# Optimization experiments

Measured on AMD Instinct MI355X. Metric: run time of the kernel, lower is better.

## Reference

```python
import jax, jax.numpy as jnp
import numpy as np
import itertools

W_ASSIGN = 1.0   # options_file['assignments_loss_weight']
W_CAT = 0.5      # options_file['categorizer_loss_weight']


def _bce(p, y):
    # torch.nn.BCELoss semantics: log terms clamped at -100
    logp = jnp.clip(jnp.log(p), -100.0)
    log1mp = jnp.clip(jnp.log1p(-p), -100.0)
    return -(y * logp + (1.0 - y) * log1mp)


def setup_inputs() -> dict:
    key = jax.random.key(0)
    k0, k1, k2, k3 = jax.random.split(key, 4)
    B, P, M = 8192, 4, 12
    assignments = jax.random.uniform(k0, (B, P, M, M), dtype=jnp.float32)
    category = jax.random.uniform(k1, (B, P), dtype=jnp.float32)
    assignments_labels = jax.random.randint(k2, (B, P, M, M), 0, 2).astype(jnp.float32)
    category_labels = jax.random.randint(k3, (B, P), 0, 2).astype(jnp.float32)
    return {
        "assignments": assignments,
        "category": category,
        "assignments_labels": assignments_labels,
        "category_labels": category_labels,
    }


def reference(assignments, category, assignments_labels, category_labels):
    B, P = assignments.shape[0], assignments.shape[1]
    # All P! permutations, in itertools order (matches first-strict-min tie-break
    # of the original loop combined with argmin's first-occurrence rule).
    perms = jnp.asarray(np.array(list(itertools.permutations(range(P))), dtype=np.int32))  # [K, P]

    # [B, K, P, M, M]: assignments with slot dim permuted for every permutation
    permuted = assignments[:, perms]
    elem = _bce(permuted, assignments_labels[:, None])          # [B, K, P, M, M]
    per_perm_loss = elem.mean(axis=(2, 3, 4))                   # [B, K]

    min_loss = per_perm_loss.min(axis=1)                        # [B]
    best = jnp.argmin(per_perm_loss, axis=1)                    # [B]
    batch_perms = perms[best]                                   # [B, P]

    permuted_category = jnp.take_along_axis(category, batch_perms, axis=1)  # [B, P]

    assignments_loss = min_loss.mean()
    category_loss = _bce(permuted_category, category_labels).mean()
    return W_ASSIGN * assignments_loss + W_CAT * category_loss
```

## Files before the change

kernel.cpp:

```cpp
#include <hip/hip_runtime.h>
#include <math.h>


#define LOG2_CLIP (-144.26950408889634f)
#define LN2F      (0.6931471805599453f)

#define PK(a,b,c,d) ((unsigned)((4u*(a)) | ((16u+4u*(b))<<8) | \
                                ((32u+4u*(c))<<16) | ((48u+4u*(d))<<24)))
__device__ const unsigned PERM_PK[32] = {
    PK(0,1,2,3), PK(0,1,3,2), PK(0,2,1,3), PK(0,2,3,1), PK(0,3,1,2), PK(0,3,2,1),
    PK(1,0,2,3), PK(1,0,3,2), PK(1,2,0,3), PK(1,2,3,0), PK(1,3,0,2), PK(1,3,2,0),
    PK(2,0,1,3), PK(2,0,3,1), PK(2,1,0,3), PK(2,1,3,0), PK(2,3,0,1), PK(2,3,1,0),
    PK(3,0,1,2), PK(3,0,2,1), PK(3,1,0,2), PK(3,1,2,0), PK(3,2,0,1), PK(3,2,1,0),
    PK(0,1,2,3), PK(0,1,2,3), PK(0,1,2,3), PK(0,1,2,3),
    PK(0,1,2,3), PK(0,1,2,3), PK(0,1,2,3), PK(0,1,2,3)
};

__global__ __launch_bounds__(256) void hsl_per_batch(
    const float* __restrict__ assign,
    const float* __restrict__ cat,
    const float* __restrict__ alabels,
    const float* __restrict__ clabels,
    float* __restrict__ ws,
    int B)
{
    const int wave = (int)((blockIdx.x * blockDim.x + threadIdx.x) >> 6);
    const int lane = (int)(threadIdx.x & 63);
    if (wave >= B) return;
    const int b = wave;

    const float* __restrict__ A = assign  + (size_t)b * 576;
    const float* __restrict__ Y = alabels + (size_t)b * 576;

    float s[16], T[4];
#pragma unroll
    for (int i = 0; i < 16; ++i) s[i] = 0.0f;
#pragma unroll
    for (int i = 0; i < 4; ++i) T[i] = 0.0f;

#pragma unroll
    for (int it = 0; it < 3; ++it) {
        if (it < 2 || lane < 16) {
            const int e = lane + it * 64;
            float d[4], y[4];
#pragma unroll
            for (int q = 0; q < 4; ++q) {
                const float a  = A[q * 144 + e];
                const float la = fmaxf(__log2f(a),        LOG2_CLIP);
                const float lb = fmaxf(__log2f(1.0f - a), LOG2_CLIP);
                d[q] = la - lb;
                T[q] += lb;
            }
#pragma unroll
            for (int p = 0; p < 4; ++p) y[p] = Y[p * 144 + e];
#pragma unroll
            for (int p = 0; p < 4; ++p)
#pragma unroll
                for (int q = 0; q < 4; ++q)
                    s[p * 4 + q] = fmaf(y[p], d[q], s[p * 4 + q]);
        }
    }
#pragma unroll
    for (int i = 0; i < 16; ++i) s[i] += T[i & 3];

    const bool h32 = (lane & 32) != 0;
    const bool h16 = (lane & 16) != 0;
    const bool h8  = (lane & 8)  != 0;
    const bool h4  = (lane & 4)  != 0;

    float t[8];
#pragma unroll
    for (int i = 0; i < 8; ++i) {
        const float keep = h32 ? s[i + 8] : s[i];
        const float send = h32 ? s[i]     : s[i + 8];
        t[i] = keep + __shfl_xor(send, 32, 64);
    }
    float u[4];
#pragma unroll
    for (int i = 0; i < 4; ++i) {
        const float keep = h16 ? t[i + 4] : t[i];
        const float send = h16 ? t[i]     : t[i + 4];
        u[i] = keep + __shfl_xor(send, 16, 64);
    }
    float w[2];
#pragma unroll
    for (int i = 0; i < 2; ++i) {
        const float keep = h8 ? u[i + 2] : u[i];
        const float send = h8 ? u[i]     : u[i + 2];
        w[i] = keep + __shfl_xor(send, 8, 64);
    }
    float x;
    {
        const float keep = h4 ? w[1] : w[0];
        const float send = h4 ? w[0] : w[1];
        x = keep + __shfl_xor(send, 4, 64);
    }
    x += __shfl_xor(x, 2, 64);
    x += __shfl_xor(x, 1, 64);

    unsigned pk = PERM_PK[lane & 31];
    const float v0 = __shfl(x, (int)( pk        & 0xFFu), 64);
    const float v1 = __shfl(x, (int)((pk >> 8)  & 0xFFu), 64);
    const float v2 = __shfl(x, (int)((pk >> 16) & 0xFFu), 64);
    const float v3 = __shfl(x, (int)( pk >> 24        ), 64);
    float score = (v0 + v1) + (v2 + v3);
    if (lane >= 24) score = -__builtin_huge_valf();

#pragma unroll
    for (int m = 16; m >= 1; m >>= 1) {
        const float    os  = __shfl_xor(score, m, 64);
        const unsigned opk = __shfl_xor(pk,    m, 64);
        const bool take = os > score;
        score = take ? os  : score;
        pk    = take ? opk : pk;
    }

    if (lane == 0) {
        const float* __restrict__ C  = cat     + (size_t)b * 4;
        const float* __restrict__ CY = clabels + (size_t)b * 4;
        float cs2 = 0.0f;
#pragma unroll
        for (int p = 0; p < 4; ++p) {
            const int q  = (int)((pk >> (8 * p + 2)) & 3u);
            const float c  = C[q];
            const float yv = CY[p];
            const float l2 = (yv != 0.0f) ? fmaxf(__log2f(c), LOG2_CLIP)
                                          : fmaxf(__log2f(1.0f - c), LOG2_CLIP);
            cs2 += l2;
        }
        ws[b] = -LN2F * (score * (1.0f / 576.0f) + 0.125f * cs2);
    }
}

__global__ __launch_bounds__(256) void hsl_reduce(
    const float* __restrict__ ws,
    float* __restrict__ out,
    int B)
{
    __shared__ double sm[256];
    double acc = 0.0;
    const int n4 = B >> 2;
    const float4* __restrict__ w4 = (const float4*)ws;
    for (int i = (int)threadIdx.x; i < n4; i += 256) {
        const float4 v = w4[i];
        acc += (double)((v.x + v.y) + (v.z + v.w));
    }
    for (int i = (n4 << 2) + (int)threadIdx.x; i < B; i += 256)
        acc += (double)ws[i];
    sm[threadIdx.x] = acc;
    __syncthreads();
    for (int r = 128; r > 0; r >>= 1) {
        if ((int)threadIdx.x < r) sm[threadIdx.x] += sm[threadIdx.x + r];
        __syncthreads();
    }
    if (threadIdx.x == 0) out[0] = (float)(sm[0] / (double)B);
}

extern "C" void kernel_launch(void* const* d_in, const int* in_sizes, int n_in,
                              void* d_out, int out_size, void* d_ws, size_t ws_size,
                              hipStream_t stream) {
    const float* assign  = (const float*)d_in[0];
    const float* cat     = (const float*)d_in[1];
    const float* alabels = (const float*)d_in[2];
    const float* clabels = (const float*)d_in[3];
    float* out = (float*)d_out;

    const int B = in_sizes[0] / 576;
    float* ws = (float*)d_ws;

    const int waves_per_block = 4;
    const int blocks = (B + waves_per_block - 1) / waves_per_block;
    hipLaunchKernelGGL(hsl_per_batch, dim3(blocks), dim3(256), 0, stream,
                       assign, cat, alabels, clabels, ws, B);
    hipLaunchKernelGGL(hsl_reduce, dim3(1), dim3(256), 0, stream,
                       ws, out, B);
}
```

Measured before the change: 16.34 us.

## Fuse per-batch loss and final reduction via fixed-point atomics, two batches per wave

Maps two batch items onto each 64-lane wave, one per 32-lane half, and adjusts the shuffle reduction and permutation lookup to match. The separate reduce kernel is removed: each 1024-thread block reduces in shared memory, adds a fixed-point 64-bit integer to a global accumulator, and the last block (found with a ticket counter) writes the output. This removes a second kernel launch and the round trip of per-batch values through the workspace, but adds a memset launch. It also assumes B is a multiple of 32 and that every per-batch value is non-negative, since negative values would wrap in the unsigned conversion.

```diff
diff --git a/kernel.cpp b/kernel.cpp
--- a/kernel.cpp
+++ b/kernel.cpp
@@ -4,9 +4,10 @@
 
 #define LOG2_CLIP (-144.26950408889634f)
 #define LN2F      (0.6931471805599453f)
+#define FIXSCALE  (4398046511104.0)
 
-#define PK(a,b,c,d) ((unsigned)((4u*(a)) | ((16u+4u*(b))<<8) | \
-                                ((32u+4u*(c))<<16) | ((48u+4u*(d))<<24)))
+#define PK(a,b,c,d) ((unsigned)((2u*(a)) | ((8u+2u*(b))<<8) | \
+                                ((16u+2u*(c))<<16) | ((24u+2u*(d))<<24)))
 __device__ const unsigned PERM_PK[32] = {
     PK(0,1,2,3), PK(0,1,3,2), PK(0,2,1,3), PK(0,2,3,1), PK(0,3,1,2), PK(0,3,2,1),
     PK(1,0,2,3), PK(1,0,3,2), PK(1,2,0,3), PK(1,2,3,0), PK(1,3,0,2), PK(1,3,2,0),
@@ -16,18 +17,23 @@
     PK(0,1,2,3), PK(0,1,2,3), PK(0,1,2,3), PK(0,1,2,3)
 };
 
-__global__ __launch_bounds__(256) void hsl_per_batch(
+__global__ __launch_bounds__(1024, 4) void hsl_fused(
     const float* __restrict__ assign,
     const float* __restrict__ cat,
     const float* __restrict__ alabels,
     const float* __restrict__ clabels,
-    float* __restrict__ ws,
-    int B)
+    unsigned long long* __restrict__ acc,
+    float* __restrict__ out,
+    int B, int nblocks)
 {
-    const int wave = (int)((blockIdx.x * blockDim.x + threadIdx.x) >> 6);
-    const int lane = (int)(threadIdx.x & 63);
-    if (wave >= B) return;
-    const int b = wave;
+    __shared__ unsigned long long lred[32];
+
+    const int tid   = (int)threadIdx.x;
+    const int wave  = tid >> 6;
+    const int lane  = tid & 63;
+    const int half  = lane >> 5;
+    const int l32   = lane & 31;
+    const int b = (int)blockIdx.x * 32 + wave * 2 + half;
 
     const float* __restrict__ A = assign  + (size_t)b * 576;
     const float* __restrict__ Y = alabels + (size_t)b * 576;
@@ -39,9 +45,9 @@
     for (int i = 0; i < 4; ++i) T[i] = 0.0f;
 
 #pragma unroll
-    for (int it = 0; it < 3; ++it) {
-        if (it < 2 || lane < 16) {
-            const int e = lane + it * 64;
+    for (int it = 0; it < 5; ++it) {
+        if (it < 4 || l32 < 16) {
+            const int e = l32 + it * 32;
             float d[4], y[4];
 #pragma unroll
             for (int q = 0; q < 4; ++q) {
@@ -63,48 +69,48 @@
 #pragma unroll
     for (int i = 0; i < 16; ++i) s[i] += T[i & 3];
 
-    const bool h32 = (lane & 32) != 0;
     const bool h16 = (lane & 16) != 0;
     const bool h8  = (lane & 8)  != 0;
     const bool h4  = (lane & 4)  != 0;
+    const bool h2  = (lane & 2)  != 0;
 
     float t[8];
 #pragma unroll
     for (int i = 0; i < 8; ++i) {
-        const float keep = h32 ? s[i + 8] : s[i];
-        const float send = h32 ? s[i]     : s[i + 8];
-        t[i] = keep + __shfl_xor(send, 32, 64);
+        const float keep = h16 ? s[i + 8] : s[i];
+        const float send = h16 ? s[i]     : s[i + 8];
+        t[i] = keep + __shfl_xor(send, 16, 64);
     }
     float u[4];
 #pragma unroll
     for (int i = 0; i < 4; ++i) {
-        const float keep = h16 ? t[i + 4] : t[i];
-        const float send = h16 ? t[i]     : t[i + 4];
-        u[i] = keep + __shfl_xor(send, 16, 64);
+        const float keep = h8 ? t[i + 4] : t[i];
+        const float send = h8 ? t[i]     : t[i + 4];
+        u[i] = keep + __shfl_xor(send, 8, 64);
     }
     float w[2];
 #pragma unroll
     for (int i = 0; i < 2; ++i) {
-        const float keep = h8 ? u[i + 2] : u[i];
-        const float send = h8 ? u[i]     : u[i + 2];
-        w[i] = keep + __shfl_xor(send, 8, 64);
+        const float keep = h4 ? u[i + 2] : u[i];
+        const float send = h4 ? u[i]     : u[i + 2];
+        w[i] = keep + __shfl_xor(send, 4, 64);
     }
     float x;
     {
-        const float keep = h4 ? w[1] : w[0];
-        const float send = h4 ? w[0] : w[1];
-        x = keep + __shfl_xor(send, 4, 64);
+        const float keep = h2 ? w[1] : w[0];
+        const float send = h2 ? w[0] : w[1];
+        x = keep + __shfl_xor(send, 2, 64);
     }
-    x += __shfl_xor(x, 2, 64);
     x += __shfl_xor(x, 1, 64);
 
-    unsigned pk = PERM_PK[lane & 31];
-    const float v0 = __shfl(x, (int)( pk        & 0xFFu), 64);
-    const float v1 = __shfl(x, (int)((pk >> 8)  & 0xFFu), 64);
-    const float v2 = __shfl(x, (int)((pk >> 16) & 0xFFu), 64);
-    const float v3 = __shfl(x, (int)( pk >> 24        ), 64);
+    unsigned pk = PERM_PK[l32];
+    const int hb = (int)(lane & 32);
+    const float v0 = __shfl(x, hb + (int)( pk        & 0xFFu), 64);
+    const float v1 = __shfl(x, hb + (int)((pk >> 8)  & 0xFFu), 64);
+    const float v2 = __shfl(x, hb + (int)((pk >> 16) & 0xFFu), 64);
+    const float v3 = __shfl(x, hb + (int)( pk >> 24        ), 64);
     float score = (v0 + v1) + (v2 + v3);
-    if (lane >= 24) score = -__builtin_huge_valf();
+    if (l32 >= 24) score = -__builtin_huge_valf();
 
 #pragma unroll
     for (int m = 16; m >= 1; m >>= 1) {
@@ -115,45 +121,39 @@
         pk    = take ? opk : pk;
     }
 
-    if (lane == 0) {
+    if (l32 == 0) {
         const float* __restrict__ C  = cat     + (size_t)b * 4;
         const float* __restrict__ CY = clabels + (size_t)b * 4;
         float cs2 = 0.0f;
 #pragma unroll
         for (int p = 0; p < 4; ++p) {
-            const int q  = (int)((pk >> (8 * p + 2)) & 3u);
+            const int q  = (int)((pk >> (8 * p + 1)) & 3u);
             const float c  = C[q];
             const float yv = CY[p];
             const float l2 = (yv != 0.0f) ? fmaxf(__log2f(c), LOG2_CLIP)
                                           : fmaxf(__log2f(1.0f - c), LOG2_CLIP);
             cs2 += l2;
         }
-        ws[b] = -LN2F * (score * (1.0f / 576.0f) + 0.125f * cs2);
+        const float val = -LN2F * (score * (1.0f / 576.0f) + 0.125f * cs2);
+        lred[tid >> 5] = (unsigned long long)((double)val * FIXSCALE + 0.5);
     }
-}
+    __syncthreads();
 
-__global__ __launch_bounds__(256) void hsl_reduce(
-    const float* __restrict__ ws,
-    float* __restrict__ out,
-    int B)
-{
-    __shared__ double sm[256];
-    double acc = 0.0;
-    const int n4 = B >> 2;
-    const float4* __restrict__ w4 = (const float4*)ws;
-    for (int i = (int)threadIdx.x; i < n4; i += 256) {
-        const float4 v = w4[i];
-        acc += (double)((v.x + v.y) + (v.z + v.w));
+    if (tid < 32) {
+        unsigned long long v = lred[tid];
+#pragma unroll
+        for (int m = 16; m >= 1; m >>= 1)
+            v += __shfl_xor(v, m, 64);
+        if (tid == 0) {
+            atomicAdd(&acc[0], v);
+            __threadfence();
+            const unsigned long long ticket = atomicAdd(&acc[1], 1ULL);
+            if (ticket == (unsigned long long)(nblocks - 1)) {
+                const unsigned long long total = atomicAdd(&acc[0], 0ULL);
+                out[0] = (float)((double)total / FIXSCALE / (double)B);
+            }
+        }
     }
-    for (int i = (n4 << 2) + (int)threadIdx.x; i < B; i += 256)
-        acc += (double)ws[i];
-    sm[threadIdx.x] = acc;
-    __syncthreads();
-    for (int r = 128; r > 0; r >>= 1) {
-        if ((int)threadIdx.x < r) sm[threadIdx.x] += sm[threadIdx.x + r];
-        __syncthreads();
-    }
-    if (threadIdx.x == 0) out[0] = (float)(sm[0] / (double)B);
 }
 
 extern "C" void kernel_launch(void* const* d_in, const int* in_sizes, int n_in,
@@ -166,12 +166,11 @@
     float* out = (float*)d_out;
 
     const int B = in_sizes[0] / 576;
-    float* ws = (float*)d_ws;
+    unsigned long long* acc = (unsigned long long*)d_ws;
 
-    const int waves_per_block = 4;
-    const int blocks = (B + waves_per_block - 1) / waves_per_block;
-    hipLaunchKernelGGL(hsl_per_batch, dim3(blocks), dim3(256), 0, stream,
-                       assign, cat, alabels, clabels, ws, B);
-    hipLaunchKernelGGL(hsl_reduce, dim3(1), dim3(256), 0, stream,
-                       ws, out, B);
+    hipMemsetAsync(acc, 0, 16, stream);
+
+    const int nblocks = B / 32;
+    hipLaunchKernelGGL(hsl_fused, dim3(nblocks), dim3(1024), 0, stream,
+                       assign, cat, alabels, clabels, acc, out, B, nblocks);
 }
```

Result: slower. 23.01 us (+40.8%).
